# Kernel optimization log

Measured on AMD Instinct MI355X. Metric: run time of the kernel, lower is better.

Reference implementation:

```python
import jax, jax.numpy as jnp
import numpy as np

B, S, EMBED, HEADS = 2, 2048, 2048, 16
HEAD_DIM = EMBED // HEADS  # 128


def setup_inputs() -> dict:
    key = jax.random.key(0)
    k1, k2, k3 = jax.random.split(key, 3)
    x = jax.random.normal(k1, (B, S, EMBED), dtype=jnp.float32)
    # qkv_proj: Linear(EMBED -> 3*EMBED, bias=False); stored as [in, out]
    w_qkv = jax.random.normal(k2, (EMBED, 3 * EMBED), dtype=jnp.float32) / np.float32(np.sqrt(EMBED))
    # out_proj: Linear(EMBED -> EMBED, bias=False)
    w_out = jax.random.normal(k3, (EMBED, EMBED), dtype=jnp.float32) / np.float32(np.sqrt(EMBED))
    return {"x": x, "w_qkv": w_qkv, "w_out": w_out}


def reference(x, w_qkv, w_out):
    b, s, e = x.shape
    h, d = HEADS, e // HEADS
    qkv = x @ w_qkv                                  # [b, s, 3e]
    q, k, v = jnp.split(qkv, 3, axis=-1)             # each [b, s, e]
    q = q.reshape(b, s, h, d).transpose(0, 2, 1, 3)  # [b, h, s, d]
    k = k.reshape(b, s, h, d).transpose(0, 2, 1, 3)
    v = v.reshape(b, s, h, d).transpose(0, 2, 1, 3)
    scale = jnp.asarray(1.0 / np.sqrt(d), dtype=q.dtype)
    scores = jnp.einsum('bhqd,bhkd->bhqk', q, k) * scale  # [b, h, s, s]
    causal = jnp.tril(jnp.ones((s, s), dtype=bool))
    scores = jnp.where(causal, scores, -jnp.inf)
    attn = jax.nn.softmax(scores, axis=-1)
    ctx = jnp.einsum('bhqk,bhkd->bhqd', attn, v)     # [b, h, s, d]
    ctx = ctx.transpose(0, 2, 1, 3).reshape(b, s, e)
    return ctx @ w_out
```

## Files before the change

kernel.cpp:

```cpp
#include <hip/hip_runtime.h>
#include <cstdint>

#define S_LEN 2048
#define EMB   2048
#define NHEAD 16
#define HDIM  128
#define MROWS 4096
#define NQKV  6144

typedef __bf16 bf16x8 __attribute__((ext_vector_type(8)));
typedef __bf16 bf16x4 __attribute__((ext_vector_type(4)));
typedef float  f32x4  __attribute__((ext_vector_type(4)));

#define MFMA16(a, b, c) __builtin_amdgcn_mfma_f32_16x16x32_bf16((a), (b), (c), 0, 0, 0)

__device__ __forceinline__ unsigned short f2bf(float f) {
  unsigned u = __builtin_bit_cast(unsigned, f);
  u += 0x7fffu + ((u >> 16) & 1u);
  return (unsigned short)(u >> 16);
}
__device__ __forceinline__ float bf2f(unsigned short u) {
  unsigned v = ((unsigned)u) << 16;
  return __builtin_bit_cast(float, v);
}

__device__ __forceinline__ void gl_lds16(const unsigned short* g, unsigned short* l) {
  __builtin_amdgcn_global_load_lds(
      (const __attribute__((address_space(1))) void*)(uintptr_t)g,
      (__attribute__((address_space(3))) void*)(unsigned int)(uintptr_t)l,
      16, 0, 0);
}

#define FENCE() asm volatile("" ::: "memory")

__global__ void cast_bf16(const float* __restrict__ in, unsigned short* __restrict__ out, int n) {
  int i = (blockIdx.x * 256 + threadIdx.x) * 4;
  if (i >= n) return;
  float4 v = *(const float4*)(in + i);
  ushort4 o;
  o.x = f2bf(v.x); o.y = f2bf(v.y); o.z = f2bf(v.z); o.w = f2bf(v.w);
  *(ushort4*)(out + i) = o;
}

__global__ void transpose_cast(const float* __restrict__ in, unsigned short* __restrict__ out,
                               int R, int C) {
  __shared__ float tile[32][33];
  int bx = blockIdx.x << 5;
  int by = blockIdx.y << 5;
  int tx = threadIdx.x, ty = threadIdx.y;
  for (int j = 0; j < 32; j += 8)
    tile[ty + j][tx] = in[(size_t)(by + ty + j) * C + bx + tx];
  __syncthreads();
  for (int j = 0; j < 32; j += 8)
    out[(size_t)(bx + ty + j) * R + by + tx] = f2bf(tile[tx][ty + j]);
}

__global__ __launch_bounds__(256, 3) void gemm_qkv(const unsigned short* __restrict__ A,
                                                   const unsigned short* __restrict__ Bt,
                                                   unsigned short* __restrict__ Qo,
                                                   unsigned short* __restrict__ Ko,
                                                   unsigned short* __restrict__ Vt) {
  __shared__ __align__(16) unsigned short As[128 * 64];
  __shared__ __align__(16) unsigned short Bs[128 * 64];
  const int tid = threadIdx.x;
  const int n0 = blockIdx.x << 7;
  const int m0 = blockIdx.y << 7;
  const int wave = tid >> 6, lane = tid & 63;
  const int wm = (wave & 1) << 6, wn = (wave >> 1) << 6;
  const int fr = lane & 15, g = lane >> 4;
  const int q = tid >> 3;
  const int jp = tid & 7;
  f32x4 acc[4][4] = {};
  for (int k0 = 0; k0 < 2048; k0 += 64) {
    for (int i = 0; i < 4; ++i) {
      const int row = q + (i << 5);
      const int jsw = (jp ^ (row & 7)) << 3;
      gl_lds16(A + (size_t)(m0 + row) * 2048 + k0 + jsw, As + (row << 6) + (jp << 3));
      gl_lds16(Bt + (size_t)(n0 + row) * 2048 + k0 + jsw, Bs + (row << 6) + (jp << 3));
    }
    __builtin_amdgcn_s_waitcnt(0);
    __syncthreads();
    for (int ks = 0; ks < 2; ++ks) {
      const int slot = (((ks << 2) + g) ^ (fr & 7)) << 3;
      bf16x8 af[4], bfv[4];
      for (int i = 0; i < 4; ++i) af[i]  = *(const bf16x8*)(As + ((wm + (i << 4) + fr) << 6) + slot);
      for (int j = 0; j < 4; ++j) bfv[j] = *(const bf16x8*)(Bs + ((wn + (j << 4) + fr) << 6) + slot);
      for (int i = 0; i < 4; ++i)
        for (int j = 0; j < 4; ++j)
          acc[i][j] = MFMA16(af[i], bfv[j], acc[i][j]);
    }
    __syncthreads();
  }
  const int which = n0 >> 11;
  const int h = (n0 >> 7) & 15;
  const int bb = m0 >> 11;
  const int bh = bb * NHEAD + h;
  for (int i = 0; i < 4; ++i) {
    const int sl = (m0 & (S_LEN - 1)) + wm + (i << 4) + (g << 2);
    for (int j = 0; j < 4; ++j) {
      const int d = wn + (j << 4) + fr;
      if (which == 2) {
        ushort4 pk;
        pk.x = f2bf(acc[i][j][0]); pk.y = f2bf(acc[i][j][1]);
        pk.z = f2bf(acc[i][j][2]); pk.w = f2bf(acc[i][j][3]);
        *(ushort4*)(Vt + ((size_t)bh * HDIM + d) * S_LEN + sl) = pk;
      } else {
        unsigned short* dst = (which == 0) ? Qo : Ko;
        for (int r = 0; r < 4; ++r)
          dst[((size_t)bh * S_LEN + sl + r) * HDIM + d] = f2bf(acc[i][j][r]);
      }
    }
  }
}

__global__ __launch_bounds__(256, 2) void attn(const unsigned short* __restrict__ Qg,
                                               const unsigned short* __restrict__ Kg,
                                               const unsigned short* __restrict__ Vtg,
                                               unsigned short* __restrict__ ctx,
                                               unsigned short* __restrict__ Opart,
                                               float* __restrict__ Lp) {
  extern __shared__ __align__(16) unsigned short lds[];
  unsigned short* KV = lds;
  unsigned short* Ps = lds + 32768;
  unsigned short* Qs = lds;

  const int blk = blockIdx.x;
  const int bh = blk & 31;
  const int t = blk >> 5;
  int qt, kt0, nkt, part;
  if (t < 8)       { qt = t;     kt0 = 0;  nkt = 2 * t + 2;       part = -1; }
  else if (t < 16) { qt = t;     kt0 = 0;  nkt = 16;              part = (bh << 3) + (qt - 8); }
  else             { qt = t - 8; kt0 = 16; nkt = 2 * qt - 14;     part = 256 + (bh << 3) + (qt - 8); }

  const int tid = threadIdx.x, wave = tid >> 6, lane = tid & 63;
  const int fr = lane & 15, g = lane >> 4;

  const unsigned short* qsrc = Qg + ((size_t)bh * S_LEN + (qt << 7)) * HDIM;
  for (int i = 0; i < 8; ++i) {
    int s0 = (i * 256 + tid) << 3;
    int q = s0 >> 7, jp = (s0 >> 3) & 15;
    gl_lds16(qsrc + (q << 7) + ((jp ^ (q & 15)) << 3), Qs + s0);
  }
  __builtin_amdgcn_s_waitcnt(0);
  __syncthreads();

  bf16x8 qf[2][4];
  for (int nbq = 0; nbq < 2; ++nbq)
    for (int kd = 0; kd < 4; ++kd) {
      int q = (wave << 5) + (nbq << 4) + fr;
      qf[nbq][kd] = *(const bf16x8*)(Qs + (q << 7) + ((((kd << 2) + g) ^ fr) << 3));
    }
  __syncthreads();

  float lsum[2] = {0.f, 0.f};
  f32x4 oacc[2][8] = {};
  const float scale = 0.08838834764831845f;

  const unsigned short* kbase = Kg + (size_t)bh * S_LEN * HDIM;
  const unsigned short* vbase = Vtg + (size_t)bh * HDIM * S_LEN;

  auto stageKV = [&](int cur, int kt) {
    const unsigned short* ks = kbase + ((size_t)kt << 6) * HDIM;
    const unsigned short* vs = vbase + (kt << 6);
    unsigned short* Kd = KV + (cur << 13);
    unsigned short* Vd = KV + 16384 + (cur << 13);
#pragma unroll
    for (int i = 0; i < 4; ++i) {
      int s0 = (i * 256 + tid) << 3;
      int key = s0 >> 7, jk = (s0 >> 3) & 15;
      gl_lds16(ks + (key << 7) + ((jk ^ (key & 15)) << 3), Kd + s0);
      int d = s0 >> 6, jv = (s0 >> 3) & 7;
      gl_lds16(vs + (size_t)d * S_LEN + ((jv ^ (d & 7)) << 3), Vd + s0);
    }
  };

  stageKV(0, kt0);

  for (int kti = 0; kti < nkt; ++kti) {
    const int cur = kti & 1;
    const int kt = kt0 + kti;
    if (kti + 1 < nkt) {
      stageKV(cur ^ 1, kt + 1);
      asm volatile("s_waitcnt vmcnt(8)" ::: "memory");
    } else {
      asm volatile("s_waitcnt vmcnt(0)" ::: "memory");
    }
    FENCE(); __builtin_amdgcn_s_barrier(); FENCE();

    const unsigned short* Kc = KV + (cur << 13);
    const unsigned short* Vc = KV + 16384 + (cur << 13);

    f32x4 sacc[2][4] = {};
    for (int kd = 0; kd < 4; ++kd)
      for (int kb = 0; kb < 4; ++kb) {
        bf16x8 kf = *(const bf16x8*)(Kc + (((kb << 4) + fr) << 7) + ((((kd << 2) + g) ^ fr) << 3));
        sacc[0][kb] = MFMA16(kf, qf[0][kd], sacc[0][kb]);
        sacc[1][kb] = MFMA16(kf, qf[1][kd], sacc[1][kb]);
      }

    const bool diag = (kt >= 2 * qt);
    for (int nbq = 0; nbq < 2; ++nbq) {
      const int qg = (qt << 7) + (wave << 5) + (nbq << 4) + fr;
      float sum = 0.f;
      for (int kb = 0; kb < 4; ++kb) {
        float p[4];
        for (int r = 0; r < 4; ++r) {
          float v = sacc[nbq][kb][r] * scale;
          if (diag) {
            int keyg = (kt << 6) + (kb << 4) + (g << 2) + r;
            if (keyg > qg) v = -__builtin_inff();
          }
          p[r] = __expf(v);
          sum += p[r];
        }
        ushort4 pk;
        pk.x = f2bf(p[0]); pk.y = f2bf(p[1]);
        pk.z = f2bf(p[2]); pk.w = f2bf(p[3]);
        *(ushort4*)(Ps + (((wave << 3) + (nbq << 2) + kb) << 8) + (lane << 2)) = pk;
      }
      lsum[nbq] += sum;
    }

    asm volatile("s_waitcnt lgkmcnt(0)" ::: "memory");
    __builtin_amdgcn_sched_barrier(0);

    for (int kc = 0; kc < 2; ++kc) {
      const int kbr = (kc << 1) + (g >> 1);
      bf16x8 ap[2];
      for (int h2 = 0; h2 < 2; ++h2) {
        const unsigned short* pb =
            Ps + (((wave << 3) + (h2 << 2) + kbr) << 8) + ((g & 1) << 7) + (fr << 2);
        bf16x4 a0 = *(const bf16x4*)pb;
        bf16x4 a1 = *(const bf16x4*)(pb + 64);
        bf16x8 a;
        a[0] = a0[0]; a[1] = a0[1]; a[2] = a0[2]; a[3] = a0[3];
        a[4] = a1[0]; a[5] = a1[1]; a[6] = a1[2]; a[7] = a1[3];
        ap[h2] = a;
      }
      for (int nd = 0; nd < 8; ++nd) {
        bf16x8 bv = *(const bf16x8*)(Vc + (((nd << 4) + fr) << 6) + ((((kc << 2) + g) ^ (fr & 7)) << 3));
        oacc[0][nd] = MFMA16(ap[0], bv, oacc[0][nd]);
        oacc[1][nd] = MFMA16(ap[1], bv, oacc[1][nd]);
      }
    }
    FENCE(); __builtin_amdgcn_s_barrier(); FENCE();
  }

  for (int nbq = 0; nbq < 2; ++nbq) {
    lsum[nbq] += __shfl_xor(lsum[nbq], 16);
    lsum[nbq] += __shfl_xor(lsum[nbq], 32);
  }

  if (part < 0) {
    const int b = bh >> 4, h = bh & 15;
    for (int mq = 0; mq < 2; ++mq)
      for (int r = 0; r < 4; ++r) {
        float lv = __shfl(lsum[mq], (lane & 48) | ((g << 2) + r));
        const float il = 1.0f / lv;
        const int s = (qt << 7) + (wave << 5) + (mq << 4) + (g << 2) + r;
        unsigned short* dst = ctx + ((size_t)(b * S_LEN + s) * EMB) + (h << 7);
        for (int nd = 0; nd < 8; ++nd)
          dst[(nd << 4) + fr] = f2bf(oacc[mq][nd][r] * il);
      }
  } else {
    unsigned short* Ob = Opart + ((size_t)part << 14);
    for (int mq = 0; mq < 2; ++mq)
      for (int r = 0; r < 4; ++r) {
        const int ql = (wave << 5) + (mq << 4) + (g << 2) + r;
        unsigned short* dst = Ob + (ql << 7);
        for (int nd = 0; nd < 8; ++nd)
          dst[(nd << 4) + fr] = f2bf(oacc[mq][nd][r]);
      }
    if (g == 0)
      for (int nbq = 0; nbq < 2; ++nbq) {
        const int ql = (wave << 5) + (nbq << 4) + fr;
        Lp[(part << 7) + ql] = lsum[nbq];
      }
  }
}

__global__ void attn_combine(const unsigned short* __restrict__ Op,
                             const float* __restrict__ Lp,
                             unsigned short* __restrict__ ctx) {
  const int tid = threadIdx.x;
  const int rid = blockIdx.x * 16 + (tid >> 4);
  const int l16 = tid & 15;
  const int bh = rid >> 10;
  const int qtl = (rid >> 7) & 7;
  const int ql = rid & 127;
  const int p = (bh << 3) + qtl;
  const float lA = Lp[(p << 7) + ql];
  const float lB = Lp[((256 + p) << 7) + ql];
  const float il = 1.0f / (lA + lB);
  const int d0 = l16 << 3;
  const unsigned short* a = Op + ((size_t)p << 14) + (ql << 7) + d0;
  const unsigned short* b = Op + ((size_t)(256 + p) << 14) + (ql << 7) + d0;
  const int bb = bh >> 4, h = bh & 15;
  const int s = ((qtl + 8) << 7) + ql;
  unsigned short* dst = ctx + ((size_t)(bb * S_LEN + s) * EMB) + (h << 7) + d0;
  ushort4 va0 = *(const ushort4*)a, va1 = *(const ushort4*)(a + 4);
  ushort4 vb0 = *(const ushort4*)b, vb1 = *(const ushort4*)(b + 4);
  ushort4 o0, o1;
  o0.x = f2bf((bf2f(va0.x) + bf2f(vb0.x)) * il);
  o0.y = f2bf((bf2f(va0.y) + bf2f(vb0.y)) * il);
  o0.z = f2bf((bf2f(va0.z) + bf2f(vb0.z)) * il);
  o0.w = f2bf((bf2f(va0.w) + bf2f(vb0.w)) * il);
  o1.x = f2bf((bf2f(va1.x) + bf2f(vb1.x)) * il);
  o1.y = f2bf((bf2f(va1.y) + bf2f(vb1.y)) * il);
  o1.z = f2bf((bf2f(va1.z) + bf2f(vb1.z)) * il);
  o1.w = f2bf((bf2f(va1.w) + bf2f(vb1.w)) * il);
  *(ushort4*)dst = o0;
  *(ushort4*)(dst + 4) = o1;
}

__device__ __forceinline__ void gemm_pipe(const unsigned short* __restrict__ Ap,
                                          const unsigned short* __restrict__ Bp,
                                          int m0, int n0, f32x4 (&acc)[4][4]) {
  extern __shared__ unsigned short glds[];
  unsigned short* As = glds;
  unsigned short* Bs = glds + 32768;
  const int tid = threadIdx.x;
  const int w = tid >> 6, lane = tid & 63;
  const int fr = lane & 15, g = lane >> 4;
  const int wm = (w >> 1) << 6;
  const int wn = (w & 1) << 6;
  const int q = tid >> 3, jp = tid & 7;

  auto stageA = [&](int buf, int kk) {
#pragma unroll
    for (int i = 0; i < 4; ++i) {
      const int row = q + (i << 6);
      gl_lds16(Ap + (size_t)(m0 + row) * 2048 + kk + ((jp ^ (row & 7)) << 3),
               As + buf * 16384 + (row << 6) + (jp << 3));
    }
  };
  auto stageB = [&](int buf, int kk) {
#pragma unroll
    for (int i = 0; i < 2; ++i) {
      const int row = q + (i << 6);
      gl_lds16(Bp + (size_t)(n0 + row) * 2048 + kk + ((jp ^ (row & 7)) << 3),
               Bs + buf * 8192 + (row << 6) + (jp << 3));
    }
  };

  stageA(0, 0); stageB(0, 0);
  int cur = 0;
#pragma unroll 2
  for (int t = 0; t < 32; ++t) {
    if (t < 31) {
      const int kn = (t + 1) << 6;
      stageA(cur ^ 1, kn); stageB(cur ^ 1, kn);
      asm volatile("s_waitcnt vmcnt(6)" ::: "memory");
    } else {
      asm volatile("s_waitcnt vmcnt(0)" ::: "memory");
    }
    __builtin_amdgcn_s_barrier();
    FENCE();

    const unsigned short* Ab = As + cur * 16384;
    const unsigned short* Bb = Bs + cur * 8192;

    bf16x8 af[4][2], bv[2][2];
#pragma unroll
    for (int i = 0; i < 4; ++i)
#pragma unroll
      for (int ks = 0; ks < 2; ++ks)
        af[i][ks] = *(const bf16x8*)(Ab + ((wm + (i << 4) + fr) << 6) +
                                     ((((ks << 2) + g) ^ (fr & 7)) << 3));
#pragma unroll
    for (int j = 0; j < 2; ++j)
#pragma unroll
      for (int ks = 0; ks < 2; ++ks)
        bv[j][ks] = *(const bf16x8*)(Bb + ((wn + (j << 4) + fr) << 6) +
                                     ((((ks << 2) + g) ^ (fr & 7)) << 3));
    __builtin_amdgcn_s_setprio(1);
#pragma unroll
    for (int ks = 0; ks < 2; ++ks)
#pragma unroll
      for (int i = 0; i < 4; ++i)
#pragma unroll
        for (int j = 0; j < 2; ++j)
          acc[i][j] = MFMA16(af[i][ks], bv[j][ks], acc[i][j]);
    __builtin_amdgcn_s_setprio(0);
    FENCE();
    __builtin_amdgcn_s_barrier();

    bf16x8 bw[2][2];
#pragma unroll
    for (int j = 0; j < 2; ++j)
#pragma unroll
      for (int ks = 0; ks < 2; ++ks)
        bw[j][ks] = *(const bf16x8*)(Bb + ((wn + ((j + 2) << 4) + fr) << 6) +
                                     ((((ks << 2) + g) ^ (fr & 7)) << 3));
    __builtin_amdgcn_s_setprio(1);
#pragma unroll
    for (int ks = 0; ks < 2; ++ks)
#pragma unroll
      for (int i = 0; i < 4; ++i)
#pragma unroll
        for (int j = 0; j < 2; ++j)
          acc[i][j + 2] = MFMA16(af[i][ks], bw[j][ks], acc[i][j + 2]);
    __builtin_amdgcn_s_setprio(0);
    FENCE();
    __builtin_amdgcn_s_barrier();
    cur ^= 1;
  }
}

__global__ __launch_bounds__(512, 2) void gemm8_out(const unsigned short* __restrict__ A,
                                                    const unsigned short* __restrict__ Bt,
                                                    float* __restrict__ C) {
  const int bid = blockIdx.x;
  const int wg = (bid & 7) * 32 + (bid >> 3);
  const int mt = wg >> 4, nt = wg & 15;
  const int m0 = mt << 8, n0 = nt << 7;
  f32x4 acc[4][4] = {};
  gemm_pipe(A, Bt, m0, n0, acc);

  const int tid = threadIdx.x, w = tid >> 6, lane = tid & 63;
  const int fr = lane & 15, g = lane >> 4;
  const int wm = (w >> 1) << 6, wn = (w & 1) << 6;
  for (int i = 0; i < 4; ++i) {
    const int row = m0 + wm + (i << 4) + (g << 2);
    for (int j = 0; j < 4; ++j) {
      const int col = n0 + wn + (j << 4) + fr;
      for (int r = 0; r < 4; ++r)
        C[(size_t)(row + r) * EMB + col] = acc[i][j][r];
    }
  }
}

extern "C" void kernel_launch(void* const* d_in, const int* in_sizes, int n_in,
                              void* d_out, int out_size, void* d_ws, size_t ws_size,
                              hipStream_t stream) {
  const float* x    = (const float*)d_in[0];
  const float* wqkv = (const float*)d_in[1];
  const float* wout = (const float*)d_in[2];
  float* out = (float*)d_out;

  unsigned short* ws = (unsigned short*)d_ws;
  const size_t NELEM = (size_t)MROWS * EMB;
  unsigned short* xb    = ws;
  unsigned short* wqkvT = xb + NELEM;
  unsigned short* woutT = wqkvT + (size_t)NQKV * EMB;
  unsigned short* Q     = woutT + (size_t)EMB * EMB;
  unsigned short* K     = Q + NELEM;
  unsigned short* Vt    = K + NELEM;
  unsigned short* ctx   = xb;
  unsigned short* Opart = wqkvT;
  float* Lp = (float*)(Opart + ((size_t)512 << 14));

  static bool attr_done = false;
  if (!attr_done) {
    (void)hipFuncSetAttribute((const void*)attn,
                              hipFuncAttributeMaxDynamicSharedMemorySize, 81920);
    (void)hipFuncSetAttribute((const void*)gemm8_out,
                              hipFuncAttributeMaxDynamicSharedMemorySize, 98304);
    attr_done = true;
  }

  cast_bf16<<<8192, 256, 0, stream>>>(x, xb, (int)NELEM);
  transpose_cast<<<dim3(NQKV / 32, EMB / 32), dim3(32, 8), 0, stream>>>(wqkv, wqkvT, EMB, NQKV);
  transpose_cast<<<dim3(EMB / 32, EMB / 32), dim3(32, 8), 0, stream>>>(wout, woutT, EMB, EMB);
  gemm_qkv<<<dim3(NQKV / 128, MROWS / 128), 256, 0, stream>>>(xb, wqkvT, Q, K, Vt);
  attn<<<768, 256, 81920, stream>>>(Q, K, Vt, ctx, Opart, Lp);
  attn_combine<<<2048, 256, 0, stream>>>(Opart, Lp, ctx);
  gemm8_out<<<256, 512, 98304, stream>>>(ctx, woutT, out);
}
```

Baseline: 358.8 us.

## Drop K/V double buffering in attention to fit three blocks per CU

The attention kernel moves from dynamic shared memory with double-buffered K/V tiles (80 KB) to static single-buffered K, V and P arrays (48 KB) and raises launch bounds to three blocks per CU. The goal is higher occupancy so that other blocks hide load latency, in place of intra-block prefetch overlap. Each iteration now waits on all loads and synchronises before compute, which exposes load latency within a block. The tighter register budget may also cause spills.

```diff
diff --git a/kernel.cpp b/kernel.cpp
--- a/kernel.cpp
+++ b/kernel.cpp
@@ -113,16 +113,17 @@
   }
 }
 
-__global__ __launch_bounds__(256, 2) void attn(const unsigned short* __restrict__ Qg,
+__global__ __launch_bounds__(256, 3) void attn(const unsigned short* __restrict__ Qg,
                                                const unsigned short* __restrict__ Kg,
                                                const unsigned short* __restrict__ Vtg,
                                                unsigned short* __restrict__ ctx,
                                                unsigned short* __restrict__ Opart,
                                                float* __restrict__ Lp) {
-  extern __shared__ __align__(16) unsigned short lds[];
-  unsigned short* KV = lds;
-  unsigned short* Ps = lds + 32768;
-  unsigned short* Qs = lds;
+  __shared__ __align__(16) unsigned short SA[16384];
+  __shared__ __align__(16) unsigned short Ps[8192];
+  unsigned short* Qs = SA;
+  unsigned short* Ks = SA;
+  unsigned short* Vs = SA + 8192;
 
   const int blk = blockIdx.x;
   const int bh = blk & 31;
@@ -159,41 +160,24 @@
   const unsigned short* kbase = Kg + (size_t)bh * S_LEN * HDIM;
   const unsigned short* vbase = Vtg + (size_t)bh * HDIM * S_LEN;
 
-  auto stageKV = [&](int cur, int kt) {
+  for (int kti = 0; kti < nkt; ++kti) {
+    const int kt = kt0 + kti;
     const unsigned short* ks = kbase + ((size_t)kt << 6) * HDIM;
     const unsigned short* vs = vbase + (kt << 6);
-    unsigned short* Kd = KV + (cur << 13);
-    unsigned short* Vd = KV + 16384 + (cur << 13);
-#pragma unroll
     for (int i = 0; i < 4; ++i) {
       int s0 = (i * 256 + tid) << 3;
       int key = s0 >> 7, jk = (s0 >> 3) & 15;
-      gl_lds16(ks + (key << 7) + ((jk ^ (key & 15)) << 3), Kd + s0);
+      gl_lds16(ks + (key << 7) + ((jk ^ (key & 15)) << 3), Ks + s0);
       int d = s0 >> 6, jv = (s0 >> 3) & 7;
-      gl_lds16(vs + (size_t)d * S_LEN + ((jv ^ (d & 7)) << 3), Vd + s0);
-    }
-  };
-
-  stageKV(0, kt0);
-
-  for (int kti = 0; kti < nkt; ++kti) {
-    const int cur = kti & 1;
-    const int kt = kt0 + kti;
-    if (kti + 1 < nkt) {
-      stageKV(cur ^ 1, kt + 1);
-      asm volatile("s_waitcnt vmcnt(8)" ::: "memory");
-    } else {
-      asm volatile("s_waitcnt vmcnt(0)" ::: "memory");
-    }
-    FENCE(); __builtin_amdgcn_s_barrier(); FENCE();
-
-    const unsigned short* Kc = KV + (cur << 13);
-    const unsigned short* Vc = KV + 16384 + (cur << 13);
+      gl_lds16(vs + (size_t)d * S_LEN + ((jv ^ (d & 7)) << 3), Vs + s0);
+    }
+    __builtin_amdgcn_s_waitcnt(0);
+    __syncthreads();
 
     f32x4 sacc[2][4] = {};
     for (int kd = 0; kd < 4; ++kd)
       for (int kb = 0; kb < 4; ++kb) {
-        bf16x8 kf = *(const bf16x8*)(Kc + (((kb << 4) + fr) << 7) + ((((kd << 2) + g) ^ fr) << 3));
+        bf16x8 kf = *(const bf16x8*)(Ks + (((kb << 4) + fr) << 7) + ((((kd << 2) + g) ^ fr) << 3));
         sacc[0][kb] = MFMA16(kf, qf[0][kd], sacc[0][kb]);
         sacc[1][kb] = MFMA16(kf, qf[1][kd], sacc[1][kb]);
       }
@@ -221,8 +205,7 @@
       lsum[nbq] += sum;
     }
 
-    asm volatile("s_waitcnt lgkmcnt(0)" ::: "memory");
-    __builtin_amdgcn_sched_barrier(0);
+    __builtin_amdgcn_s_waitcnt(0);
 
     for (int kc = 0; kc < 2; ++kc) {
       const int kbr = (kc << 1) + (g >> 1);
@@ -238,12 +221,12 @@
         ap[h2] = a;
       }
       for (int nd = 0; nd < 8; ++nd) {
-        bf16x8 bv = *(const bf16x8*)(Vc + (((nd << 4) + fr) << 6) + ((((kc << 2) + g) ^ (fr & 7)) << 3));
+        bf16x8 bv = *(const bf16x8*)(Vs + (((nd << 4) + fr) << 6) + ((((kc << 2) + g) ^ (fr & 7)) << 3));
         oacc[0][nd] = MFMA16(ap[0], bv, oacc[0][nd]);
         oacc[1][nd] = MFMA16(ap[1], bv, oacc[1][nd]);
       }
     }
-    FENCE(); __builtin_amdgcn_s_barrier(); FENCE();
+    __syncthreads();
   }
 
   for (int nbq = 0; nbq < 2; ++nbq) {
@@ -452,8 +435,6 @@
 
   static bool attr_done = false;
   if (!attr_done) {
-    (void)hipFuncSetAttribute((const void*)attn,
-                              hipFuncAttributeMaxDynamicSharedMemorySize, 81920);
     (void)hipFuncSetAttribute((const void*)gemm8_out,
                               hipFuncAttributeMaxDynamicSharedMemorySize, 98304);
     attr_done = true;
@@ -463,7 +444,7 @@
   transpose_cast<<<dim3(NQKV / 32, EMB / 32), dim3(32, 8), 0, stream>>>(wqkv, wqkvT, EMB, NQKV);
   transpose_cast<<<dim3(EMB / 32, EMB / 32), dim3(32, 8), 0, stream>>>(wout, woutT, EMB, EMB);
   gemm_qkv<<<dim3(NQKV / 128, MROWS / 128), 256, 0, stream>>>(xb, wqkvT, Q, K, Vt);
-  attn<<<768, 256, 81920, stream>>>(Q, K, Vt, ctx, Opart, Lp);
+  attn<<<768, 256, 0, stream>>>(Q, K, Vt, ctx, Opart, Lp);
   attn_combine<<<2048, 256, 0, stream>>>(Opart, Lp, ctx);
   gemm8_out<<<256, 512, 98304, stream>>>(ctx, woutT, out);
 }
```

Result: slower. 367.1 us (+2.3%).
